# Kernel optimization log

Measured on AMD Instinct MI355X. Metric: run time of the kernel, lower is better.

The kernel has to match this reference:

```python
import math
import jax, jax.numpy as jnp
import numpy as np

N_ORDERS = 2
CHUNK = 64  # tokens per chunk (before virtual-token expansion)


def _expand_derivative(x, n):
    """expand_virtual_tokens(mode='derivative'): [B,H,S,D] -> [B,H,S*n,D]."""
    B, H, S, D = x.shape
    pad = jnp.zeros((B, H, n - 1, D), x.dtype)
    xp = jnp.concatenate([pad, x], axis=2)  # [B,H,S+n-1,D]
    coeffs = np.array([(-1) ** kk * math.comb(n - 1, kk) for kk in range(n)], dtype=np.float32)
    coeffs = coeffs / np.abs(coeffs).sum()  # L1-normalized binomial coeffs
    # window j at token t is x_pad[t+j]*coeffs[j]; then flip window dim (as in torch .flip(-1))
    win = jnp.stack([xp[:, :, j:j + S, :] * coeffs[j] for j in range(n)], axis=3)  # [B,H,S,n,D]
    win = win[:, :, :, ::-1, :]
    return win.reshape(B, H, S * n, D)


def _unlinear(x, scale=2.0):
    """unlinear_activation: gated norm-scaled gelu applied to inter-chunk state."""
    xn = jnp.linalg.norm(x, axis=-1, keepdims=True) + 1e-6
    return x / scale * jax.nn.gelu(scale * x / xn, approximate=True)


def _stab(x):
    # ensure_stability: clamp to [-1e4, 1e4], nan -> center (0)
    return jnp.nan_to_num(jnp.clip(x, -1e4, 1e4), nan=0.0, posinf=1e4, neginf=-1e4)


def _forward(q, k, v, beta):
    n = N_ORDERS
    B, H, S, D = q.shape
    qe = _expand_derivative(q, n)
    ke = _expand_derivative(k, n)
    ve = _expand_derivative(v, n)
    be = jnp.repeat(beta, n, axis=-1)[..., None]  # [B,H,S*n,1]
    w = ke * be  # delta-rule write keys
    u = ve * be  # delta-rule write values

    Cn = CHUNK * n                     # virtual tokens per chunk
    NC = (S * n) // Cn                 # number of chunks
    ch = lambda x: x.reshape(B, H, NC, Cn, D)
    qc, kc, wc, uc = ch(qe), ch(ke), ch(w), ch(u)

    # triangular (forward-substitution) inversion per chunk:
    # T = (I + tril(W K^T, -1))^{-1}  == fast_invert_matrix of the strictly-lower system
    A = jnp.tril(jnp.einsum('bhnid,bhnjd->bhnij', wc, kc), -1)
    eye = jnp.eye(Cn, dtype=q.dtype)
    T = jax.scipy.linalg.solve_triangular(
        eye + A, jnp.broadcast_to(eye, A.shape), lower=True, unit_diagonal=True)
    wci = jnp.einsum('bhnij,bhnjd->bhnid', T, wc)
    uci = jnp.einsum('bhnij,bhnjd->bhnid', T, uc)

    def chunk_step(h, xs):
        # sequential_delta_product_scan body: per-token Householder updates, n_orders steps
        qx, wx, ux = xs  # each [B,H,Cn,D]
        C = CHUNK
        qr = qx.reshape(B, H, C, n, D)
        wr = wx.reshape(B, H, C, n, D)
        ur = ux.reshape(B, H, C, n, D)
        state = jnp.broadcast_to(h[:, :, None], (B, H, C, D, D))  # per-token state
        outs = []
        for s in range(n):
            qs, ws, us = qr[:, :, :, s], wr[:, :, :, s], ur[:, :, :, s]
            kho = jnp.einsum('bhcd,bhcde->bhce', ws, state)
            uval = us - kho
            o_inter = jnp.einsum('bhcd,bhcde->bhce', qs, state)
            o_intra = qs * uval
            state = _stab(state + jnp.einsum('bhcd,bhce->bhcde', ws, uval))
            outs.append(o_intra + o_inter)
        o = jnp.stack(outs, axis=3).reshape(B, H, C * n, D)  # interleave: pos t*n+s
        h_new = _unlinear(state[:, :, -1])  # linear_activation=False path
        return h_new, o

    xs = (jnp.moveaxis(qc, 2, 0), jnp.moveaxis(wci, 2, 0), jnp.moveaxis(uci, 2, 0))
    h0 = jnp.zeros((B, H, D, D), q.dtype)
    _, os = jax.lax.scan(chunk_step, h0, xs)  # os: [NC,B,H,Cn,D]
    out_v = jnp.moveaxis(os, 0, 2).reshape(B, H, S, n, D)
    return out_v[..., n - 1, :]  # collapse virtual tokens: keep last-order output per token


def setup_inputs() -> dict:
    key = jax.random.key(0)
    kq, kk, kv, kb = jax.random.split(key, 4)
    B, H, S, D = 2, 16, 2048, 64
    return {
        'q': jax.random.normal(kq, (B, H, S, D), jnp.float32),
        'k': jax.random.normal(kk, (B, H, S, D), jnp.float32),
        'v': jax.random.normal(kv, (B, H, S, D), jnp.float32),
        'beta': jax.random.uniform(kb, (B, H, S), jnp.float32),
    }


def reference(q, k, v, beta):
    return _forward(q, k, v, beta)
```

## Files before the change

### kernel.cpp

```cpp
#include <hip/hip_runtime.h>
#include <math.h>


namespace {
constexpr int PAIRS = 32;
constexpr int SLEN  = 2048;
constexpr int D     = 64;
constexpr int CK    = 64;
constexpr int CN    = 128;
constexpr int NCH   = 32;
constexpr int NB2   = 16;
constexpr int NP    = 5;
constexpr size_t YWORDS = (size_t)PAIRS * NCH * CN * CN;
constexpr int GP = 2145;
constexpr size_t GGW = (size_t)PAIRS * NCH * GP;
constexpr size_t HGW = (size_t)PAIRS * (NCH + 1) * D * D;

__device__ __forceinline__ float stab1(float x) {
    float y = __builtin_amdgcn_fmed3f(x, -10000.f, 10000.f);
    return (x != x) ? 0.f : y;
}

__device__ __forceinline__ int kidx(int a, int f4) {
    return a * 68 + 4 * (f4 ^ ((a >> 2) & 3));
}

__device__ __forceinline__ void bar_lds() {
    asm volatile("s_waitcnt lgkmcnt(0)\n\ts_barrier" ::: "memory");
}
}

__global__ __launch_bounds__(256, 2)
void la_gram(const float* __restrict__ kg, float* __restrict__ gG)
{
    __shared__ float kstf[65 * 68];
    const int blk = blockIdx.x;
    const int p = blk >> 5, nc = blk & 31;
    const int tid = threadIdx.x;
    const int baseT = nc * CK;
    const float* kp = kg + (size_t)p * SLEN * D;

    for (int u = tid; u < 65 * 16; u += 256) {
        int a = u >> 4, f4 = u & 15;
        int src = baseT - 1 + a;
        float4 val = float4{0.f, 0.f, 0.f, 0.f};
        if (src >= 0) val = ((const float4*)(kp + (size_t)src * D))[f4];
        *(float4*)&kstf[kidx(a, f4)] = val;
    }
    __syncthreads();

    float* gps = gG + (size_t)blk * GP;
    for (int tt = tid; tt < 17 * 17; tt += 256) {
        int ta = tt / 17, tb = tt % 17;
        if (tb > ta) continue;
        int a0 = ta * 4, b0 = tb * 4;
        float acc[4][4] = {};
        for (int d4 = 0; d4 < 16; ++d4) {
            float4 av[4], bv[4];
            #pragma unroll
            for (int r = 0; r < 4; ++r) {
                av[r] = *(const float4*)&kstf[kidx(min(a0 + r, 64), d4)];
                bv[r] = *(const float4*)&kstf[kidx(min(b0 + r, 64), d4)];
            }
            #pragma unroll
            for (int r = 0; r < 4; ++r)
                #pragma unroll
                for (int c = 0; c < 4; ++c)
                    acc[r][c] += av[r].x * bv[c].x + av[r].y * bv[c].y
                               + av[r].z * bv[c].z + av[r].w * bv[c].w;
        }
        #pragma unroll
        for (int r = 0; r < 4; ++r)
            #pragma unroll
            for (int c = 0; c < 4; ++c) {
                int a = a0 + r, b = b0 + c;
                if (a <= 64 && b <= a)
                    gps[a * (a + 1) / 2 + b] = acc[r][c];
            }
    }
}

__global__ __launch_bounds__(256, 3)
void la_phase1g(const float* __restrict__ kg, const float* __restrict__ vg,
                const float* __restrict__ bg, float* __restrict__ ws,
                const float* __restrict__ gG)
{
    __shared__ float Ysh[CN][64];
    __shared__ float scm[2][CN][8];
    __shared__ float redsh[24][66];
    __shared__ float bq4[CK], bh[CK];

    const int blk  = blockIdx.x;
    const int p    = blk >> 6;
    const int nc   = (blk >> 1) & 31;
    const int half = blk & 1;
    const int tid  = threadIdx.x;
    const int col  = tid & 63;
    const int m    = tid >> 6;
    const int baseT = nc * CK;
    const float* kp = kg + (size_t)p * SLEN * D;
    const float* vp = vg + (size_t)p * SLEN * D;
    const float* bp = bg + (size_t)p * SLEN;
    const float* gps = gG + (size_t)(p * NCH + nc) * GP;

    if (tid < CK) {
        float bv = bp[baseT + tid];
        bq4[tid] = 0.25f * bv;
        bh[tid]  = 0.5f  * bv;
    }
    __syncthreads();

    const float* srcBase = half ? vp : kp;
    for (int u = tid; u < CN * 16; u += 256) {
        int i = u >> 4, f4 = u & 15;
        int ci = i >> 1, si = i & 1;
        float sc = si ? bh[ci] : -bh[ci];
        int srcT = baseT + ci - si;
        float4 val = float4{0.f, 0.f, 0.f, 0.f};
        if (srcT >= 0) val = ((const float4*)(srcBase + (size_t)srcT * D))[f4];
        val.x *= sc; val.y *= sc; val.z *= sc; val.w *= sc;
        *(float4*)&Ysh[i][f4 * 4] = val;
    }
    for (int e = tid; e < 64; e += 256) {
        int j = e >> 3, r = e & 7;
        int ai = (r >> 1) - (r & 1) + 1;
        int aj = (j >> 1) - (j & 1) + 1;
        int amax = max(ai, aj), amin = min(ai, aj);
        float sgn = ((r ^ j) & 1) ? -1.f : 1.f;
        scm[0][j][r] = sgn * bq4[r >> 1] * gps[amax * (amax + 1) / 2 + amin];
    }
    __syncthreads();

    #pragma unroll
    for (int g = 0; g < 16; ++g) {
        const int buf = g & 1;
        float acc[8] = {};
        #pragma unroll
        for (int jj = 0; jj < 2 * g; ++jj) {
            const int j = m + 4 * jj;
            float yv = Ysh[j][col];
            const float4 a03 = *(const float4*)&scm[buf][j][0];
            const float4 a47 = *(const float4*)&scm[buf][j][4];
            acc[0] += a03.x * yv; acc[1] += a03.y * yv;
            acc[2] += a03.z * yv; acc[3] += a03.w * yv;
            acc[4] += a47.x * yv; acc[5] += a47.y * yv;
            acc[6] += a47.z * yv; acc[7] += a47.w * yv;
        }
        if (m > 0) {
            #pragma unroll
            for (int r = 0; r < 8; ++r) redsh[(m - 1) * 8 + r][col] = acc[r];
        }
        bar_lds();
        if (m == 0) {
            if (g > 0) {
                #pragma unroll
                for (int r = 0; r < 8; ++r)
                    acc[r] += redsh[r][col] + redsh[8 + r][col] + redsh[16 + r][col];
            }
            float yn[8];
            #pragma unroll
            for (int r = 0; r < 8; ++r) {
                float val = Ysh[8 * g + r][col] - acc[r];
                #pragma unroll
                for (int rp = 0; rp < 8; ++rp)
                    if (rp < r) val -= scm[buf][8 * g + rp][r] * yn[rp];
                yn[r] = val;
                Ysh[8 * g + r][col] = val;
            }
        } else if (g < 15) {
            const int T = g + 1, bufB = T & 1;
            const int nel = 8 * (8 * T + 8);
            constexpr int MAXIT = 6;
            const int nit = (nel + 191) / 192;
            #pragma unroll
            for (int it = 0; it < MAXIT; ++it) {
                if (it < nit) {
                    const int e = (tid - 64) + 192 * it;
                    if (e < nel) {
                        int j = e >> 3, r = e & 7;
                        int i = 8 * T + r;
                        int ai = (i >> 1) - (i & 1) + 1;
                        int aj = (j >> 1) - (j & 1) + 1;
                        int amax = max(ai, aj), amin = min(ai, aj);
                        float sgn = ((i ^ j) & 1) ? -1.f : 1.f;
                        scm[bufB][j][r] =
                            sgn * bq4[i >> 1] * gps[amax * (amax + 1) / 2 + amin];
                    }
                }
            }
        }
        bar_lds();
    }

    float* gY = ws + (size_t)(p * NCH + nc) * (CN * CN) + half * 64;
    for (int u = tid; u < CN * 16; u += 256) {
        int r = u >> 4, f4 = u & 15;
        *(float4*)&gY[r * CN + f4 * 4] = *(const float4*)&Ysh[r][f4 * 4];
    }
}

__global__ __launch_bounds__(512, 1)
void la_scan(const float* __restrict__ ws, float* __restrict__ hg)
{
    __shared__ float w0s[64], u0s[64], w1s[64], u1s[64];
    __shared__ float pA[8][64], pB[8][64];
    __shared__ float hsh2[64][67];

    const int p = blockIdx.x;
    const int tid = threadIdx.x;
    const int w = tid >> 6, lane = tid & 63;
    const int hd = tid >> 3, he0 = (tid & 7) * 8;
    const float* Yp = ws + (size_t)p * NCH * (CN * CN);
    float* hp = hg + (size_t)p * (NCH + 1) * (D * D);

    for (int idx = tid; idx < D * D; idx += 512) hp[idx] = 0.f;
    for (int idx = tid; idx < 64 * 67; idx += 512) (&hsh2[0][0])[idx] = 0.f;

    auto stagew = [&](float v) {
        if (tid < 64)       w0s[tid] = v;
        else if (tid < 128) u0s[tid - 64] = v;
        else if (tid < 192) w1s[tid - 128] = v;
        else if (tid < 256) u1s[tid - 192] = v;
    };
    {
        float v = 0.f;
        if (tid < 256) v = Yp[(size_t)(126 + (tid >> 7)) * CN + (tid & 127)];
        stagew(v);
    }
    float hs[8];
    #pragma unroll
    for (int j = 0; j < 8; ++j) hs[j] = 0.f;
    __syncthreads();

    for (int nc = 0; nc < NCH; ++nc) {
        float pf = 0.f;
        if (nc + 1 < NCH && tid < 256)
            pf = Yp[(size_t)(nc + 1) * (CN * CN)
                    + (size_t)(126 + (tid >> 7)) * CN + (tid & 127)];

        float s = 0.f;
        #pragma unroll
        for (int j = 0; j < 8; ++j) s += w0s[8 * w + j] * hs[j];
        pA[w][lane] = s;
        bar_lds();

        float sum = 0.f;
        #pragma unroll
        for (int wv = 0; wv < 8; ++wv) sum += pA[wv][lane];
        const float uv0 = u0s[lane] - sum;

        float st1[8];
        float s2 = 0.f;
        #pragma unroll
        for (int j = 0; j < 8; ++j) {
            st1[j] = stab1(hs[j] + w0s[8 * w + j] * uv0);
            s2 += w1s[8 * w + j] * st1[j];
        }
        pB[w][lane] = s2;
        bar_lds();

        float sum2 = 0.f;
        #pragma unroll
        for (int wv = 0; wv < 8; ++wv) sum2 += pB[wv][lane];
        const float uv1 = u1s[lane] - sum2;
        #pragma unroll
        for (int j = 0; j < 8; ++j)
            hsh2[8 * w + j][lane] = stab1(st1[j] + w1s[8 * w + j] * uv1);
        bar_lds();

        {
            float st2v[8];
            float ssum = 0.f;
            #pragma unroll
            for (int j = 0; j < 8; ++j) {
                st2v[j] = hsh2[hd][he0 + j];
                ssum += st2v[j] * st2v[j];
            }
            ssum += __shfl_xor(ssum, 1);
            ssum += __shfl_xor(ssum, 2);
            ssum += __shfl_xor(ssum, 4);
            float xn = __builtin_amdgcn_sqrtf(ssum) + 1e-6f;
            float sc2 = 2.f * __builtin_amdgcn_rcpf(xn);
            float hn[8];
            #pragma unroll
            for (int j = 0; j < 8; ++j) {
                float x  = st2v[j];
                float y  = x * sc2;
                float y2 = y * y;
                float e  = __builtin_amdgcn_exp2f(y * (2.3022078f + 0.1029432f * y2));
                float th = (e - 1.f) * __builtin_amdgcn_rcpf(e + 1.f);
                hn[j] = 0.25f * x * y * (1.f + th);
                hsh2[hd][he0 + j] = hn[j];
            }
            float* ho = hp + (size_t)(nc + 1) * (D * D) + hd * 64 + he0;
            *(float4*)&ho[0] = float4{hn[0], hn[1], hn[2], hn[3]};
            *(float4*)&ho[4] = float4{hn[4], hn[5], hn[6], hn[7]};
        }
        if (nc + 1 < NCH) stagew(pf);
        bar_lds();
        #pragma unroll
        for (int j = 0; j < 8; ++j) hs[j] = hsh2[8 * w + j][lane];
    }
}

__global__ __launch_bounds__(512)
void la_out(const float* __restrict__ qg, const float* __restrict__ ws,
            const float* __restrict__ hg, float* __restrict__ outg)
{
    __shared__ float hT[64 * 68];
    __shared__ float wbr[8][3][64];

    const int blk = blockIdx.x;
    const int p = blk >> 5, nc = blk & 31;
    const int tid = threadIdx.x;
    const int w = tid >> 6, lane = tid & 63;

    const float* Yc = ws + (size_t)(p * NCH + nc) * (CN * CN);
    const float* hp = hg + ((size_t)p * (NCH + 1) + nc) * (D * D);
    const float* qp = qg + (size_t)p * SLEN * D;
    float* op = outg + (size_t)p * SLEN * D;

    for (int idx = tid; idx < D * D; idx += 512) {
        int d = idx >> 6, e = idx & 63;
        hT[e * 68 + d] = hp[idx];
    }
    __syncthreads();

    float4 hr[16];
    #pragma unroll
    for (int k = 0; k < 16; ++k)
        hr[k] = *(const float4*)&hT[lane * 68 + 4 * k];

    float w0n, u0n, w1n, u1n, qn;
    {
        const int c = w, t = nc * CK + c;
        w0n = Yc[(size_t)(2 * c) * CN + lane];
        u0n = Yc[(size_t)(2 * c) * CN + 64 + lane];
        w1n = Yc[(size_t)(2 * c + 1) * CN + lane];
        u1n = Yc[(size_t)(2 * c + 1) * CN + 64 + lane];
        qn  = qp[(size_t)((t > 0) ? t - 1 : 0) * D + lane];
    }

    for (int it = 0; it < 8; ++it) {
        const int c = it * 8 + w;
        const int t = nc * CK + c;
        const float w0v = w0n, u0l = u0n, w1v = w1n, u1l = u1n, qv = qn;
        if (it < 7) {
            const int c2 = (it + 1) * 8 + w;
            w0n = Yc[(size_t)(2 * c2) * CN + lane];
            u0n = Yc[(size_t)(2 * c2) * CN + 64 + lane];
            w1n = Yc[(size_t)(2 * c2 + 1) * CN + lane];
            u1n = Yc[(size_t)(2 * c2 + 1) * CN + 64 + lane];
            qn  = qp[(size_t)(nc * CK + c2 - 1) * D + lane];
        }

        wbr[w][0][lane] = w0v;
        wbr[w][1][lane] = w1v;
        wbr[w][2][lane] = qv;

        float uv0 = u0l;
        #pragma unroll
        for (int k = 0; k < 16; ++k) {
            float4 wb = *(const float4*)&wbr[w][0][4 * k];
            uv0 -= (wb.x * hr[k].x + wb.y * hr[k].y)
                 + (wb.z * hr[k].z + wb.w * hr[k].w);
        }
        float kh = 0.f, oa = 0.f;
        #pragma unroll
        for (int k = 0; k < 16; ++k) {
            float4 wb0 = *(const float4*)&wbr[w][0][4 * k];
            float4 wb1 = *(const float4*)&wbr[w][1][4 * k];
            float4 qb  = *(const float4*)&wbr[w][2][4 * k];
            float st0 = stab1(hr[k].x + wb0.x * uv0);
            float st1 = stab1(hr[k].y + wb0.y * uv0);
            float st2 = stab1(hr[k].z + wb0.z * uv0);
            float st3 = stab1(hr[k].w + wb0.w * uv0);
            kh += (wb1.x * st0 + wb1.y * st1) + (wb1.z * st2 + wb1.w * st3);
            oa += (qb.x * st0 + qb.y * st1) + (qb.z * st2 + qb.w * st3);
        }
        float uv1 = u1l - kh;
        float outv = 0.5f * (qv * uv1 + oa);
        op[(size_t)t * D + lane] = (t > 0) ? outv : 0.f;
    }
}

__global__ __launch_bounds__(256, 2)
void la_phase1f(const float* __restrict__ kg, const float* __restrict__ vg,
                const float* __restrict__ bg, float* __restrict__ ws)
{
    __shared__ float Ysh[CN][64];
    __shared__ float Gm[65][66];
    __shared__ char  ureg[17680];
    __shared__ float bq4[CK], bh[CK];

    float* kstf = (float*)ureg;
    float* scm  = (float*)ureg;
    float (*redsh)[66] = (float(*)[66])(ureg + 8192);

    const int blk  = blockIdx.x;
    const int p    = blk >> 6;
    const int nc   = (blk >> 1) & 31;
    const int half = blk & 1;
    const int tid  = threadIdx.x;
    const int baseT = nc * CK;
    const float* kp = kg + (size_t)p * SLEN * D;
    const float* vp = vg + (size_t)p * SLEN * D;
    const float* bp = bg + (size_t)p * SLEN;

    for (int u = tid; u < 65 * 16; u += 256) {
        int a = u >> 4, f4 = u & 15;
        int src = baseT - 1 + a;
        float4 val = float4{0.f, 0.f, 0.f, 0.f};
        if (src >= 0) val = ((const float4*)(kp + (size_t)src * D))[f4];
        *(float4*)&kstf[kidx(a, f4)] = val;
    }
    if (tid < CK) {
        float bv = bp[baseT + tid];
        bq4[tid] = 0.25f * bv;
        bh[tid]  = 0.5f  * bv;
    }
    __syncthreads();

    for (int u = tid; u < CN * 16; u += 256) {
        int i = u >> 4, f4 = u & 15;
        int ci = i >> 1, si = i & 1;
        float sc = si ? bh[ci] : -bh[ci];
        float4 val = float4{0.f, 0.f, 0.f, 0.f};
        if (half == 0) {
            val = *(const float4*)&kstf[kidx(ci - si + 1, f4)];
        } else {
            int srcT = baseT + ci - si;
            if (srcT >= 0) val = ((const float4*)(vp + (size_t)srcT * D))[f4];
        }
        val.x *= sc; val.y *= sc; val.z *= sc; val.w *= sc;
        *(float4*)&Ysh[i][f4 * 4] = val;
    }

    for (int tt = tid; tt < 17 * 17; tt += 256) {
        int ta = tt / 17, tb = tt % 17;
        if (tb > ta) continue;
        int a0 = ta * 4, b0 = tb * 4;
        float acc[4][4] = {};
        for (int d4 = 0; d4 < 16; ++d4) {
            float4 av[4], bv[4];
            #pragma unroll
            for (int r = 0; r < 4; ++r) {
                av[r] = *(const float4*)&kstf[kidx(min(a0 + r, 64), d4)];
                bv[r] = *(const float4*)&kstf[kidx(min(b0 + r, 64), d4)];
            }
            #pragma unroll
            for (int r = 0; r < 4; ++r)
                #pragma unroll
                for (int c = 0; c < 4; ++c)
                    acc[r][c] += av[r].x * bv[c].x + av[r].y * bv[c].y
                               + av[r].z * bv[c].z + av[r].w * bv[c].w;
        }
        #pragma unroll
        for (int r = 0; r < 4; ++r)
            #pragma unroll
            for (int c = 0; c < 4; ++c)
                if (a0 + r <= 64 && b0 + c <= 64) {
                    Gm[a0 + r][b0 + c] = acc[r][c];
                    Gm[b0 + c][a0 + r] = acc[r][c];
                }
    }
    __syncthreads();

    auto stripf = [&](int g, int t0, int tstride) {
        int buf = g & 1;
        int jmax = 8 * g + 8;
        for (int e = t0; e < 8 * jmax; e += tstride) {
            int j = e >> 3, r = e & 7;
            int i = 8 * g + r;
            int ai = (i >> 1) - (i & 1) + 1;
            int aj = (j >> 1) - (j & 1) + 1;
            float sgn = ((i ^ j) & 1) ? -1.f : 1.f;
            scm[(buf * CN + j) * 8 + r] = sgn * bq4[i >> 1] * Gm[ai][aj];
        }
    };

    stripf(0, tid, 256);
    __syncthreads();

    const int col = tid & 63;
    const int m   = tid >> 6;
    for (int g = 0; g < 16; ++g) {
        const int buf = g & 1;
        float acc[8] = {};
        for (int j = m; j < 8 * g; j += 4) {
            float yv = Ysh[j][col];
            const float4 a03 = *(const float4*)&scm[(buf * CN + j) * 8];
            const float4 a47 = *(const float4*)&scm[(buf * CN + j) * 8 + 4];
            acc[0] += a03.x * yv; acc[1] += a03.y * yv;
            acc[2] += a03.z * yv; acc[3] += a03.w * yv;
            acc[4] += a47.x * yv; acc[5] += a47.y * yv;
            acc[6] += a47.z * yv; acc[7] += a47.w * yv;
        }
        if (m > 0) {
            #pragma unroll
            for (int r = 0; r < 8; ++r) redsh[(m - 1) * 8 + r][col] = acc[r];
        }
        __syncthreads();
        if (m == 0) {
            if (g > 0) {
                #pragma unroll
                for (int r = 0; r < 8; ++r)
                    acc[r] += redsh[r][col] + redsh[8 + r][col] + redsh[16 + r][col];
            }
            float yn[8];
            #pragma unroll
            for (int r = 0; r < 8; ++r) {
                float val = Ysh[8 * g + r][col] - acc[r];
                #pragma unroll
                for (int rp = 0; rp < 8; ++rp)
                    if (rp < r) val -= scm[(buf * CN + 8 * g + rp) * 8 + r] * yn[rp];
                yn[r] = val;
                Ysh[8 * g + r][col] = val;
            }
        } else if (g < 15) {
            stripf(g + 1, tid - 64, 192);
        }
        __syncthreads();
    }

    float* gY = ws + (size_t)(p * NCH + nc) * (CN * CN) + half * 64;
    for (int u = tid; u < CN * 16; u += 256) {
        int r = u >> 4, f4 = u & 15;
        *(float4*)&gY[r * CN + f4 * 4] = *(const float4*)&Ysh[r][f4 * 4];
    }
}

__global__ __launch_bounds__(512, 4)
void la_phase2(const float* __restrict__ qg, const float* __restrict__ ws,
               float* __restrict__ outg)
{
    __shared__ float WU[2][NP][256];
    __shared__ float Qs[2][NP][64];
    __shared__ float pR1[8][NP][64];
    __shared__ float pKH[8][NP][64];
    __shared__ float pOA[8][NP][64];
    __shared__ float UV0[NP][64];
    __shared__ float UV1r[64];
    __shared__ float hsh[64][67];

    const int blk  = blockIdx.x;
    const int p    = blk >> 4, nb = blk & 15;
    const int tid  = threadIdx.x;
    const int w    = tid >> 6, lane = tid & 63;
    const int hd   = tid >> 3;
    const int he0  = (tid & 7) * 8;

    const float* qp = qg + (size_t)p * SLEN * D;
    float* op = outg + (size_t)p * SLEN * D;
    const float* wsbase = ws + (size_t)p * NCH * (CN * CN);

    const int cMain = nb * 4 + w;

    float4 wuR = float4{0.f, 0.f, 0.f, 0.f};
    float  qR  = 0.f;

    auto stage_load = [&](int nc) {
        const float* gY = wsbase + (size_t)nc * (CN * CN);
        if (w < 4) {
            wuR = *(const float4*)(gY + (size_t)(2 * cMain) * CN + lane * 4);
            int t = nc * CK + cMain;
            qR = qp[(size_t)((t > 0) ? t - 1 : 0) * D + lane];
        } else if (w == 4) {
            wuR = *(const float4*)(gY + (size_t)126 * CN + lane * 4);
            qR = qp[(size_t)(nc * CK + 62) * D + lane];
        }
    };
    auto stage_write = [&](int buf) {
        if (w < NP) {
            *(float4*)&WU[buf][w][lane * 4] = wuR;
            Qs[buf][w][lane] = qR;
        }
    };

    for (int idx = tid; idx < 64 * 67; idx += 512) (&hsh[0][0])[idx] = 0.f;
    stage_load(0);
    stage_write(0);
    __syncthreads();

    for (int nc = 0; nc < NCH; ++nc) {
        const int buf = nc & 1;
        float hs[8];
        #pragma unroll
        for (int j = 0; j < 8; ++j) hs[j] = hsh[8 * w + j][lane];
        if (nc + 1 < NCH) stage_load(nc + 1);

        #pragma unroll
        for (int P = 0; P < NP; ++P) {
            float4 a = *(const float4*)&WU[buf][P][8 * w];
            float4 b = *(const float4*)&WU[buf][P][8 * w + 4];
            pR1[w][P][lane] =
                  ((a.x * hs[0] + a.y * hs[1]) + (a.z * hs[2] + a.w * hs[3]))
                + ((b.x * hs[4] + b.y * hs[5]) + (b.z * hs[6] + b.w * hs[7]));
        }
        __syncthreads();

        if (w < NP) {
            float s = 0.f;
            #pragma unroll
            for (int wv = 0; wv < 8; ++wv) s += pR1[wv][w][lane];
            UV0[w][lane] = WU[buf][w][64 + lane] - s;
        }
        __syncthreads();

        #pragma unroll
        for (int P = 0; P < NP; ++P) {
            float uv0 = UV0[P][lane];
            float4 w0a = *(const float4*)&WU[buf][P][8 * w];
            float4 w0b = *(const float4*)&WU[buf][P][8 * w + 4];
            float4 w1a = *(const float4*)&WU[buf][P][128 + 8 * w];
            float4 w1b = *(const float4*)&WU[buf][P][128 + 8 * w + 4];
            float4 qa  = *(const float4*)&Qs[buf][P][8 * w];
            float4 qb  = *(const float4*)&Qs[buf][P][8 * w + 4];
            float st0 = stab1(hs[0] + w0a.x * uv0);
            float st1 = stab1(hs[1] + w0a.y * uv0);
            float st2 = stab1(hs[2] + w0a.z * uv0);
            float st3 = stab1(hs[3] + w0a.w * uv0);
            float st4 = stab1(hs[4] + w0b.x * uv0);
            float st5 = stab1(hs[5] + w0b.y * uv0);
            float st6 = stab1(hs[6] + w0b.z * uv0);
            float st7 = stab1(hs[7] + w0b.w * uv0);
            pKH[w][P][lane] =
                  ((w1a.x * st0 + w1a.y * st1) + (w1a.z * st2 + w1a.w * st3))
                + ((w1b.x * st4 + w1b.y * st5) + (w1b.z * st6 + w1b.w * st7));
            pOA[w][P][lane] =
                  ((qa.x * st0 + qa.y * st1) + (qa.z * st2 + qa.w * st3))
                + ((qb.x * st4 + qb.y * st5) + (qb.z * st6 + qb.w * st7));
        }
        stage_write(buf ^ 1);
        __syncthreads();

        if (w < 4) {
            float skh = 0.f, soa = 0.f;
            #pragma unroll
            for (int wv = 0; wv < 8; ++wv) {
                skh += pKH[wv][w][lane];
                soa += pOA[wv][w][lane];
            }
            float uv1 = WU[buf][w][192 + lane] - skh;
            int t = nc * CK + cMain;
            float outv = 0.5f * (Qs[buf][w][lane] * uv1 + soa);
            op[(size_t)t * D + lane] = (t > 0) ? outv : 0.f;
        } else if (w == 4) {
            float skh = 0.f;
            #pragma unroll
            for (int wv = 0; wv < 8; ++wv) skh += pKH[wv][4][lane];
            UV1r[lane] = WU[buf][4][192 + lane] - skh;
        }
        __syncthreads();

        {
            float w0d = WU[buf][4][hd];
            float w1d = WU[buf][4][128 + hd];
            float st2v[8];
            float ssum = 0.f;
            #pragma unroll
            for (int j = 0; j < 8; ++j) {
                float st1 = stab1(hsh[hd][he0 + j] + w0d * UV0[4][he0 + j]);
                float st2 = stab1(st1 + w1d * UV1r[he0 + j]);
                st2v[j] = st2;
                ssum += st2 * st2;
            }
            ssum += __shfl_xor(ssum, 1);
            ssum += __shfl_xor(ssum, 2);
            ssum += __shfl_xor(ssum, 4);
            float xn = __builtin_amdgcn_sqrtf(ssum) + 1e-6f;
            float s2 = 2.f * __builtin_amdgcn_rcpf(xn);
            #pragma unroll
            for (int j = 0; j < 8; ++j) {
                float x  = st2v[j];
                float y  = x * s2;
                float y2 = y * y;
                float e  = __builtin_amdgcn_exp2f(y * (2.3022078f + 0.1029432f * y2));
                float th = (e - 1.f) * __builtin_amdgcn_rcpf(e + 1.f);
                hsh[hd][he0 + j] = 0.25f * x * y * (1.f + th);
            }
        }
        __syncthreads();
    }
}

extern "C" void kernel_launch(void* const* d_in, const int* in_sizes, int n_in,
                              void* d_out, int out_size, void* d_ws, size_t ws_size,
                              hipStream_t stream)
{
    (void)in_sizes; (void)n_in; (void)out_size;
    const float* q    = (const float*)d_in[0];
    const float* k    = (const float*)d_in[1];
    const float* v    = (const float*)d_in[2];
    const float* beta = (const float*)d_in[3];
    float* ws  = (float*)d_ws;
    float* out = (float*)d_out;

    const size_t maxW  = (HGW > GGW) ? HGW : GGW;
    const size_t needA = (YWORDS + maxW) * sizeof(float);
    const size_t needB = (YWORDS + GGW) * sizeof(float);

    if (ws_size >= needA) {
        float* gG = ws + YWORDS;
        float* hg = ws + YWORDS;
        la_gram<<<PAIRS * NCH, 256, 0, stream>>>(k, gG);
        la_phase1g<<<PAIRS * NCH * 2, 256, 0, stream>>>(k, v, beta, ws, gG);
        la_scan<<<PAIRS, 512, 0, stream>>>(ws, hg);
        la_out<<<PAIRS * NCH, 512, 0, stream>>>(q, ws, hg, out);
    } else if (ws_size >= needB) {
        float* gG = ws + YWORDS;
        la_gram<<<PAIRS * NCH, 256, 0, stream>>>(k, gG);
        la_phase1g<<<PAIRS * NCH * 2, 256, 0, stream>>>(k, v, beta, ws, gG);
        la_phase2<<<PAIRS * NB2, 512, 0, stream>>>(q, ws, out);
    } else {
        la_phase1f<<<PAIRS * NCH * 2, 256, 0, stream>>>(k, v, beta, ws);
        la_phase2<<<PAIRS * NB2, 512, 0, stream>>>(q, ws, out);
    }
}
```

Measured before the change: 260.5 us.

## Fuse per-chunk solve and inter-chunk scan into one kernel with flag handoff

Merges the chunk-wise triangular solve (phase1g) and the sequential state scan into a single launch. The first PAIRS blocks run the scan and spin on per-chunk atomic flags, while the remaining blocks compute chunk Y matrices (ordered by chunk index) and signal completion with release atomics. This lets the serial scan start as soon as early chunks are ready instead of waiting for the whole phase, and drops one kernel launch. In exchange it adds a memset, relies on scan blocks being co-resident with producers to avoid deadlock, and runs the scan with 256 threads instead of 512.

```diff
diff --git a/kernel.cpp b/kernel.cpp
--- a/kernel.cpp
+++ b/kernel.cpp
@@ -15,16 +15,15 @@
 constexpr int GP = 2145;
 constexpr size_t GGW = (size_t)PAIRS * NCH * GP;
 constexpr size_t HGW = (size_t)PAIRS * (NCH + 1) * D * D;
+constexpr size_t FLW = PAIRS * NCH;
 
 __device__ __forceinline__ float stab1(float x) {
     float y = __builtin_amdgcn_fmed3f(x, -10000.f, 10000.f);
     return (x != x) ? 0.f : y;
 }
-
 __device__ __forceinline__ int kidx(int a, int f4) {
     return a * 68 + 4 * (f4 ^ ((a >> 2) & 3));
 }
-
 __device__ __forceinline__ void bar_lds() {
     asm volatile("s_waitcnt lgkmcnt(0)\n\ts_barrier" ::: "memory");
 }
@@ -81,20 +80,128 @@
 }
 
 __global__ __launch_bounds__(256, 3)
-void la_phase1g(const float* __restrict__ kg, const float* __restrict__ vg,
-                const float* __restrict__ bg, float* __restrict__ ws,
-                const float* __restrict__ gG)
+void la_p1scan(const float* __restrict__ kg, const float* __restrict__ vg,
+               const float* __restrict__ bg, float* __restrict__ ws,
+               const float* __restrict__ gG, float* __restrict__ hg,
+               unsigned int* __restrict__ flags)
 {
-    __shared__ float Ysh[CN][64];
-    __shared__ float scm[2][CN][8];
-    __shared__ float redsh[24][66];
-    __shared__ float bq4[CK], bh[CK];
-
-    const int blk  = blockIdx.x;
-    const int p    = blk >> 6;
-    const int nc   = (blk >> 1) & 31;
-    const int half = blk & 1;
-    const int tid  = threadIdx.x;
+    __shared__ char shm[47808];
+    const int blk = blockIdx.x;
+    const int tid = threadIdx.x;
+
+    if (blk < PAIRS) {
+        float* w0s = (float*)shm;
+        float* u0s = w0s + 64;
+        float* w1s = u0s + 64;
+        float* u1s = w1s + 64;
+        float (*pA)[64] = (float(*)[64])(u1s + 64);
+        float (*pB)[64] = pA + 4;
+        float (*hsh2)[67] = (float(*)[67])(pB + 4);
+
+        const int p = blk;
+        const int w = tid >> 6, lane = tid & 63;
+        const int hd = tid >> 2, he0 = (tid & 3) * 16;
+        const float* Yp = ws + (size_t)p * NCH * (CN * CN);
+        float* hp = hg + (size_t)p * (NCH + 1) * (D * D);
+        const unsigned int* fl = (const unsigned int*)flags + (size_t)p * NCH;
+
+        for (int idx = tid; idx < D * D; idx += 256) hp[idx] = 0.f;
+
+        float hs[16];
+        #pragma unroll
+        for (int j = 0; j < 16; ++j) hs[j] = 0.f;
+
+        for (int nc = 0; nc < NCH; ++nc) {
+            if (tid == 0) {
+                while (__hip_atomic_load(&fl[nc], __ATOMIC_ACQUIRE,
+                                         __HIP_MEMORY_SCOPE_AGENT) < 2u)
+                    __builtin_amdgcn_s_sleep(16);
+            }
+            __syncthreads();
+
+            {
+                float v = Yp[(size_t)nc * (CN * CN)
+                             + (size_t)(126 + (tid >> 7)) * CN + (tid & 127)];
+                if (tid < 64)       w0s[tid] = v;
+                else if (tid < 128) u0s[tid - 64] = v;
+                else if (tid < 192) w1s[tid - 128] = v;
+                else                u1s[tid - 192] = v;
+            }
+            bar_lds();
+
+            float s = 0.f;
+            #pragma unroll
+            for (int j = 0; j < 16; ++j) s += w0s[16 * w + j] * hs[j];
+            pA[w][lane] = s;
+            bar_lds();
+
+            float sum = pA[0][lane] + pA[1][lane] + pA[2][lane] + pA[3][lane];
+            const float uv0 = u0s[lane] - sum;
+
+            float st1[16];
+            float s2 = 0.f;
+            #pragma unroll
+            for (int j = 0; j < 16; ++j) {
+                st1[j] = stab1(hs[j] + w0s[16 * w + j] * uv0);
+                s2 += w1s[16 * w + j] * st1[j];
+            }
+            pB[w][lane] = s2;
+            bar_lds();
+
+            float sum2 = pB[0][lane] + pB[1][lane] + pB[2][lane] + pB[3][lane];
+            const float uv1 = u1s[lane] - sum2;
+            #pragma unroll
+            for (int j = 0; j < 16; ++j)
+                hsh2[16 * w + j][lane] = stab1(st1[j] + w1s[16 * w + j] * uv1);
+            bar_lds();
+
+            {
+                float st2v[16];
+                float ssum = 0.f;
+                #pragma unroll
+                for (int j = 0; j < 16; ++j) {
+                    st2v[j] = hsh2[hd][he0 + j];
+                    ssum += st2v[j] * st2v[j];
+                }
+                ssum += __shfl_xor(ssum, 1);
+                ssum += __shfl_xor(ssum, 2);
+                float xn = __builtin_amdgcn_sqrtf(ssum) + 1e-6f;
+                float sc2 = 2.f * __builtin_amdgcn_rcpf(xn);
+                float* ho = hp + (size_t)(nc + 1) * (D * D) + hd * 64 + he0;
+                #pragma unroll
+                for (int j4 = 0; j4 < 4; ++j4) {
+                    float hn[4];
+                    #pragma unroll
+                    for (int q = 0; q < 4; ++q) {
+                        float x  = st2v[4 * j4 + q];
+                        float y  = x * sc2;
+                        float y2 = y * y;
+                        float e  = __builtin_amdgcn_exp2f(
+                                       y * (2.3022078f + 0.1029432f * y2));
+                        float th = (e - 1.f) * __builtin_amdgcn_rcpf(e + 1.f);
+                        hn[q] = 0.25f * x * y * (1.f + th);
+                        hsh2[hd][he0 + 4 * j4 + q] = hn[q];
+                    }
+                    *(float4*)&ho[4 * j4] = float4{hn[0], hn[1], hn[2], hn[3]};
+                }
+            }
+            bar_lds();
+            #pragma unroll
+            for (int j = 0; j < 16; ++j) hs[j] = hsh2[16 * w + j][lane];
+        }
+        return;
+    }
+
+    float (*Ysh)[64]   = (float(*)[64])shm;
+    float (*scm)[CN][8] = (float(*)[CN][8])(shm + 32768);
+    float (*redsh)[66] = (float(*)[66])(shm + 40960);
+    float* bq4 = (float*)(shm + 47296);
+    float* bh  = bq4 + 64;
+
+    const int idx  = blk - PAIRS;
+    const int nc   = idx >> 6;
+    const int p    = (idx & 63) >> 1;
+    const int half = idx & 1;
     const int col  = tid & 63;
     const int m    = tid >> 6;
     const int baseT = nc * CK;
@@ -197,110 +304,10 @@
         int r = u >> 4, f4 = u & 15;
         *(float4*)&gY[r * CN + f4 * 4] = *(const float4*)&Ysh[r][f4 * 4];
     }
-}
-
-__global__ __launch_bounds__(512, 1)
-void la_scan(const float* __restrict__ ws, float* __restrict__ hg)
-{
-    __shared__ float w0s[64], u0s[64], w1s[64], u1s[64];
-    __shared__ float pA[8][64], pB[8][64];
-    __shared__ float hsh2[64][67];
-
-    const int p = blockIdx.x;
-    const int tid = threadIdx.x;
-    const int w = tid >> 6, lane = tid & 63;
-    const int hd = tid >> 3, he0 = (tid & 7) * 8;
-    const float* Yp = ws + (size_t)p * NCH * (CN * CN);
-    float* hp = hg + (size_t)p * (NCH + 1) * (D * D);
-
-    for (int idx = tid; idx < D * D; idx += 512) hp[idx] = 0.f;
-    for (int idx = tid; idx < 64 * 67; idx += 512) (&hsh2[0][0])[idx] = 0.f;
-
-    auto stagew = [&](float v) {
-        if (tid < 64)       w0s[tid] = v;
-        else if (tid < 128) u0s[tid - 64] = v;
-        else if (tid < 192) w1s[tid - 128] = v;
-        else if (tid < 256) u1s[tid - 192] = v;
-    };
-    {
-        float v = 0.f;
-        if (tid < 256) v = Yp[(size_t)(126 + (tid >> 7)) * CN + (tid & 127)];
-        stagew(v);
-    }
-    float hs[8];
-    #pragma unroll
-    for (int j = 0; j < 8; ++j) hs[j] = 0.f;
-    __syncthreads();
-
-    for (int nc = 0; nc < NCH; ++nc) {
-        float pf = 0.f;
-        if (nc + 1 < NCH && tid < 256)
-            pf = Yp[(size_t)(nc + 1) * (CN * CN)
-                    + (size_t)(126 + (tid >> 7)) * CN + (tid & 127)];
-
-        float s = 0.f;
-        #pragma unroll
-        for (int j = 0; j < 8; ++j) s += w0s[8 * w + j] * hs[j];
-        pA[w][lane] = s;
-        bar_lds();
-
-        float sum = 0.f;
-        #pragma unroll
-        for (int wv = 0; wv < 8; ++wv) sum += pA[wv][lane];
-        const float uv0 = u0s[lane] - sum;
-
-        float st1[8];
-        float s2 = 0.f;
-        #pragma unroll
-        for (int j = 0; j < 8; ++j) {
-            st1[j] = stab1(hs[j] + w0s[8 * w + j] * uv0);
-            s2 += w1s[8 * w + j] * st1[j];
-        }
-        pB[w][lane] = s2;
-        bar_lds();
-
-        float sum2 = 0.f;
-        #pragma unroll
-        for (int wv = 0; wv < 8; ++wv) sum2 += pB[wv][lane];
-        const float uv1 = u1s[lane] - sum2;
-        #pragma unroll
-        for (int j = 0; j < 8; ++j)
-            hsh2[8 * w + j][lane] = stab1(st1[j] + w1s[8 * w + j] * uv1);
-        bar_lds();
-
-        {
-            float st2v[8];
-            float ssum = 0.f;
-            #pragma unroll
-            for (int j = 0; j < 8; ++j) {
-                st2v[j] = hsh2[hd][he0 + j];
-                ssum += st2v[j] * st2v[j];
-            }
-            ssum += __shfl_xor(ssum, 1);
-            ssum += __shfl_xor(ssum, 2);
-            ssum += __shfl_xor(ssum, 4);
-            float xn = __builtin_amdgcn_sqrtf(ssum) + 1e-6f;
-            float sc2 = 2.f * __builtin_amdgcn_rcpf(xn);
-            float hn[8];
-            #pragma unroll
-            for (int j = 0; j < 8; ++j) {
-                float x  = st2v[j];
-                float y  = x * sc2;
-                float y2 = y * y;
-                float e  = __builtin_amdgcn_exp2f(y * (2.3022078f + 0.1029432f * y2));
-                float th = (e - 1.f) * __builtin_amdgcn_rcpf(e + 1.f);
-                hn[j] = 0.25f * x * y * (1.f + th);
-                hsh2[hd][he0 + j] = hn[j];
-            }
-            float* ho = hp + (size_t)(nc + 1) * (D * D) + hd * 64 + he0;
-            *(float4*)&ho[0] = float4{hn[0], hn[1], hn[2], hn[3]};
-            *(float4*)&ho[4] = float4{hn[4], hn[5], hn[6], hn[7]};
-        }
-        if (nc + 1 < NCH) stagew(pf);
-        bar_lds();
-        #pragma unroll
-        for (int j = 0; j < 8; ++j) hs[j] = hsh2[8 * w + j][lane];
-    }
+    __syncthreads();
+    if (tid == 0)
+        __hip_atomic_fetch_add(&flags[p * NCH + nc], 1u, __ATOMIC_RELEASE,
+                               __HIP_MEMORY_SCOPE_AGENT);
 }
 
 __global__ __launch_bounds__(512)
@@ -381,6 +388,229 @@
         float uv1 = u1l - kh;
         float outv = 0.5f * (qv * uv1 + oa);
         op[(size_t)t * D + lane] = (t > 0) ? outv : 0.f;
+    }
+}
+
+__global__ __launch_bounds__(256, 3)
+void la_phase1g(const float* __restrict__ kg, const float* __restrict__ vg,
+                const float* __restrict__ bg, float* __restrict__ ws,
+                const float* __restrict__ gG)
+{
+    __shared__ float Ysh[CN][64];
+    __shared__ float scm[2][CN][8];
+    __shared__ float redsh[24][66];
+    __shared__ float bq4[CK], bh[CK];
+
+    const int blk  = blockIdx.x;
+    const int p    = blk >> 6;
+    const int nc   = (blk >> 1) & 31;
+    const int half = blk & 1;
+    const int tid  = threadIdx.x;
+    const int col  = tid & 63;
+    const int m    = tid >> 6;
+    const int baseT = nc * CK;
+    const float* kp = kg + (size_t)p * SLEN * D;
+    const float* vp = vg + (size_t)p * SLEN * D;
+    const float* bp = bg + (size_t)p * SLEN;
+    const float* gps = gG + (size_t)(p * NCH + nc) * GP;
+
+    if (tid < CK) {
+        float bv = bp[baseT + tid];
+        bq4[tid] = 0.25f * bv;
+        bh[tid]  = 0.5f  * bv;
+    }
+    __syncthreads();
+
+    const float* srcBase = half ? vp : kp;
+    for (int u = tid; u < CN * 16; u += 256) {
+        int i = u >> 4, f4 = u & 15;
+        int ci = i >> 1, si = i & 1;
+        float sc = si ? bh[ci] : -bh[ci];
+        int srcT = baseT + ci - si;
+        float4 val = float4{0.f, 0.f, 0.f, 0.f};
+        if (srcT >= 0) val = ((const float4*)(srcBase + (size_t)srcT * D))[f4];
+        val.x *= sc; val.y *= sc; val.z *= sc; val.w *= sc;
+        *(float4*)&Ysh[i][f4 * 4] = val;
+    }
+    for (int e = tid; e < 64; e += 256) {
+        int j = e >> 3, r = e & 7;
+        int ai = (r >> 1) - (r & 1) + 1;
+        int aj = (j >> 1) - (j & 1) + 1;
+        int amax = max(ai, aj), amin = min(ai, aj);
+        float sgn = ((r ^ j) & 1) ? -1.f : 1.f;
+        scm[0][j][r] = sgn * bq4[r >> 1] * gps[amax * (amax + 1) / 2 + amin];
+    }
+    __syncthreads();
+
+    #pragma unroll
+    for (int g = 0; g < 16; ++g) {
+        const int buf = g & 1;
+        float acc[8] = {};
+        #pragma unroll
+        for (int jj = 0; jj < 2 * g; ++jj) {
+            const int j = m + 4 * jj;
+            float yv = Ysh[j][col];
+            const float4 a03 = *(const float4*)&scm[buf][j][0];
+            const float4 a47 = *(const float4*)&scm[buf][j][4];
+            acc[0] += a03.x * yv; acc[1] += a03.y * yv;
+            acc[2] += a03.z * yv; acc[3] += a03.w * yv;
+            acc[4] += a47.x * yv; acc[5] += a47.y * yv;
+            acc[6] += a47.z * yv; acc[7] += a47.w * yv;
+        }
+        if (m > 0) {
+            #pragma unroll
+            for (int r = 0; r < 8; ++r) redsh[(m - 1) * 8 + r][col] = acc[r];
+        }
+        bar_lds();
+        if (m == 0) {
+            if (g > 0) {
+                #pragma unroll
+                for (int r = 0; r < 8; ++r)
+                    acc[r] += redsh[r][col] + redsh[8 + r][col] + redsh[16 + r][col];
+            }
+            float yn[8];
+            #pragma unroll
+            for (int r = 0; r < 8; ++r) {
+                float val = Ysh[8 * g + r][col] - acc[r];
+                #pragma unroll
+                for (int rp = 0; rp < 8; ++rp)
+                    if (rp < r) val -= scm[buf][8 * g + rp][r] * yn[rp];
+                yn[r] = val;
+                Ysh[8 * g + r][col] = val;
+            }
+        } else if (g < 15) {
+            const int T = g + 1, bufB = T & 1;
+            const int nel = 8 * (8 * T + 8);
+            constexpr int MAXIT = 6;
+            const int nit = (nel + 191) / 192;
+            #pragma unroll
+            for (int it = 0; it < MAXIT; ++it) {
+                if (it < nit) {
+                    const int e = (tid - 64) + 192 * it;
+                    if (e < nel) {
+                        int j = e >> 3, r = e & 7;
+                        int i = 8 * T + r;
+                        int ai = (i >> 1) - (i & 1) + 1;
+                        int aj = (j >> 1) - (j & 1) + 1;
+                        int amax = max(ai, aj), amin = min(ai, aj);
+                        float sgn = ((i ^ j) & 1) ? -1.f : 1.f;
+                        scm[bufB][j][r] =
+                            sgn * bq4[i >> 1] * gps[amax * (amax + 1) / 2 + amin];
+                    }
+                }
+            }
+        }
+        bar_lds();
+    }
+
+    float* gY = ws + (size_t)(p * NCH + nc) * (CN * CN) + half * 64;
+    for (int u = tid; u < CN * 16; u += 256) {
+        int r = u >> 4, f4 = u & 15;
+        *(float4*)&gY[r * CN + f4 * 4] = *(const float4*)&Ysh[r][f4 * 4];
+    }
+}
+
+__global__ __launch_bounds__(512, 1)
+void la_scan(const float* __restrict__ ws, float* __restrict__ hg)
+{
+    __shared__ float w0s[64], u0s[64], w1s[64], u1s[64];
+    __shared__ float pA[8][64], pB[8][64];
+    __shared__ float hsh2[64][67];
+
+    const int p = blockIdx.x;
+    const int tid = threadIdx.x;
+    const int w = tid >> 6, lane = tid & 63;
+    const int hd = tid >> 3, he0 = (tid & 7) * 8;
+    const float* Yp = ws + (size_t)p * NCH * (CN * CN);
+    float* hp = hg + (size_t)p * (NCH + 1) * (D * D);
+
+    for (int idx = tid; idx < D * D; idx += 512) hp[idx] = 0.f;
+    for (int idx = tid; idx < 64 * 67; idx += 512) (&hsh2[0][0])[idx] = 0.f;
+
+    auto stagew = [&](float v) {
+        if (tid < 64)       w0s[tid] = v;
+        else if (tid < 128) u0s[tid - 64] = v;
+        else if (tid < 192) w1s[tid - 128] = v;
+        else if (tid < 256) u1s[tid - 192] = v;
+    };
+    {
+        float v = 0.f;
+        if (tid < 256) v = Yp[(size_t)(126 + (tid >> 7)) * CN + (tid & 127)];
+        stagew(v);
+    }
+    float hs[8];
+    #pragma unroll
+    for (int j = 0; j < 8; ++j) hs[j] = 0.f;
+    __syncthreads();
+
+    for (int nc = 0; nc < NCH; ++nc) {
+        float pf = 0.f;
+        if (nc + 1 < NCH && tid < 256)
+            pf = Yp[(size_t)(nc + 1) * (CN * CN)
+                    + (size_t)(126 + (tid >> 7)) * CN + (tid & 127)];
+
+        float s = 0.f;
+        #pragma unroll
+        for (int j = 0; j < 8; ++j) s += w0s[8 * w + j] * hs[j];
+        pA[w][lane] = s;
+        bar_lds();
+
+        float sum = 0.f;
+        #pragma unroll
+        for (int wv = 0; wv < 8; ++wv) sum += pA[wv][lane];
+        const float uv0 = u0s[lane] - sum;
+
+        float st1[8];
+        float s2 = 0.f;
+        #pragma unroll
+        for (int j = 0; j < 8; ++j) {
+            st1[j] = stab1(hs[j] + w0s[8 * w + j] * uv0);
+            s2 += w1s[8 * w + j] * st1[j];
+        }
+        pB[w][lane] = s2;
+        bar_lds();
+
+        float sum2 = 0.f;
+        #pragma unroll
+        for (int wv = 0; wv < 8; ++wv) sum2 += pB[wv][lane];
+        const float uv1 = u1s[lane] - sum2;
+        #pragma unroll
+        for (int j = 0; j < 8; ++j)
+            hsh2[8 * w + j][lane] = stab1(st1[j] + w1s[8 * w + j] * uv1);
+        bar_lds();
+
+        {
+            float st2v[8];
+            float ssum = 0.f;
+            #pragma unroll
+            for (int j = 0; j < 8; ++j) {
+                st2v[j] = hsh2[hd][he0 + j];
+                ssum += st2v[j] * st2v[j];
+            }
+            ssum += __shfl_xor(ssum, 1);
+            ssum += __shfl_xor(ssum, 2);
+            ssum += __shfl_xor(ssum, 4);
+            float xn = __builtin_amdgcn_sqrtf(ssum) + 1e-6f;
+            float sc2 = 2.f * __builtin_amdgcn_rcpf(xn);
+            float hn[8];
+            #pragma unroll
+            for (int j = 0; j < 8; ++j) {
+                float x  = st2v[j];
+                float y  = x * sc2;
+                float y2 = y * y;
+                float e  = __builtin_amdgcn_exp2f(y * (2.3022078f + 0.1029432f * y2));
+                float th = (e - 1.f) * __builtin_amdgcn_rcpf(e + 1.f);
+                hn[j] = 0.25f * x * y * (1.f + th);
+                hsh2[hd][he0 + j] = hn[j];
+            }
+            float* ho = hp + (size_t)(nc + 1) * (D * D) + hd * 64 + he0;
+            *(float4*)&ho[0] = float4{hn[0], hn[1], hn[2], hn[3]};
+            *(float4*)&ho[4] = float4{hn[4], hn[5], hn[6], hn[7]};
+        }
+        if (nc + 1 < NCH) stagew(pf);
+        bar_lds();
+        #pragma unroll
+        for (int j = 0; j < 8; ++j) hs[j] = hsh2[8 * w + j][lane];
     }
 }
 
@@ -697,10 +927,20 @@
     float* out = (float*)d_out;
 
     const size_t maxW  = (HGW > GGW) ? HGW : GGW;
+    const size_t needF = (YWORDS + GGW + HGW + FLW) * sizeof(float);
     const size_t needA = (YWORDS + maxW) * sizeof(float);
     const size_t needB = (YWORDS + GGW) * sizeof(float);
 
-    if (ws_size >= needA) {
+    if (ws_size >= needF) {
+        float* gG = ws + YWORDS;
+        float* hg = gG + GGW;
+        unsigned int* flags = (unsigned int*)(hg + HGW);
+        hipMemsetAsync(flags, 0, FLW * sizeof(unsigned int), stream);
+        la_gram<<<PAIRS * NCH, 256, 0, stream>>>(k, gG);
+        la_p1scan<<<PAIRS + PAIRS * NCH * 2, 256, 0, stream>>>(
+            k, v, beta, ws, gG, hg, (unsigned int*)flags);
+        la_out<<<PAIRS * NCH, 512, 0, stream>>>(q, ws, hg, out);
+    } else if (ws_size >= needA) {
         float* gG = ws + YWORDS;
         float* hg = ws + YWORDS;
         la_gram<<<PAIRS * NCH, 256, 0, stream>>>(k, gG);
```

After: 292.7 us. 12.3% more time.

## Fuse scan and output kernels with per-chunk flags to overlap them

Applied to the files above, without the earlier changes.

The sequential state scan and the per-chunk output computation are merged into one launch. The first 32 blocks run the scan and publish a release flag after each chunk's state is written. The remaining blocks spin on an acquire load of their chunk's flag before reading that state. Output work for early chunks can now overlap the serial scan instead of waiting for the whole scan kernel to finish. In exchange the change adds a memset launch and spin-waiting, and it relies on the scan blocks being scheduled before or alongside the waiting blocks to avoid deadlock.

```diff
diff --git a/kernel.cpp b/kernel.cpp
--- a/kernel.cpp
+++ b/kernel.cpp
@@ -15,16 +15,15 @@
 constexpr int GP = 2145;
 constexpr size_t GGW = (size_t)PAIRS * NCH * GP;
 constexpr size_t HGW = (size_t)PAIRS * (NCH + 1) * D * D;
+constexpr size_t FLW2 = (size_t)PAIRS * NCH;
 
 __device__ __forceinline__ float stab1(float x) {
     float y = __builtin_amdgcn_fmed3f(x, -10000.f, 10000.f);
     return (x != x) ? 0.f : y;
 }
-
 __device__ __forceinline__ int kidx(int a, int f4) {
     return a * 68 + 4 * (f4 ^ ((a >> 2) & 3));
 }
-
 __device__ __forceinline__ void bar_lds() {
     asm volatile("s_waitcnt lgkmcnt(0)\n\ts_barrier" ::: "memory");
 }
@@ -199,126 +198,148 @@
     }
 }
 
-__global__ __launch_bounds__(512, 1)
-void la_scan(const float* __restrict__ ws, float* __restrict__ hg)
+__global__ __launch_bounds__(512)
+void la_scanout(const float* __restrict__ qg, const float* __restrict__ ws,
+                float* __restrict__ hg, float* __restrict__ outg,
+                unsigned int* __restrict__ flags)
 {
-    __shared__ float w0s[64], u0s[64], w1s[64], u1s[64];
-    __shared__ float pA[8][64], pB[8][64];
-    __shared__ float hsh2[64][67];
-
-    const int p = blockIdx.x;
+    __shared__ char shm[23808];
+    const int blk = blockIdx.x;
     const int tid = threadIdx.x;
-    const int w = tid >> 6, lane = tid & 63;
-    const int hd = tid >> 3, he0 = (tid & 7) * 8;
-    const float* Yp = ws + (size_t)p * NCH * (CN * CN);
-    float* hp = hg + (size_t)p * (NCH + 1) * (D * D);
-
-    for (int idx = tid; idx < D * D; idx += 512) hp[idx] = 0.f;
-    for (int idx = tid; idx < 64 * 67; idx += 512) (&hsh2[0][0])[idx] = 0.f;
-
-    auto stagew = [&](float v) {
-        if (tid < 64)       w0s[tid] = v;
-        else if (tid < 128) u0s[tid - 64] = v;
-        else if (tid < 192) w1s[tid - 128] = v;
-        else if (tid < 256) u1s[tid - 192] = v;
-    };
-    {
-        float v = 0.f;
-        if (tid < 256) v = Yp[(size_t)(126 + (tid >> 7)) * CN + (tid & 127)];
-        stagew(v);
-    }
-    float hs[8];
-    #pragma unroll
-    for (int j = 0; j < 8; ++j) hs[j] = 0.f;
-    __syncthreads();
-
-    for (int nc = 0; nc < NCH; ++nc) {
-        float pf = 0.f;
-        if (nc + 1 < NCH && tid < 256)
-            pf = Yp[(size_t)(nc + 1) * (CN * CN)
-                    + (size_t)(126 + (tid >> 7)) * CN + (tid & 127)];
-
-        float s = 0.f;
-        #pragma unroll
-        for (int j = 0; j < 8; ++j) s += w0s[8 * w + j] * hs[j];
-        pA[w][lane] = s;
-        bar_lds();
-
-        float sum = 0.f;
-        #pragma unroll
-        for (int wv = 0; wv < 8; ++wv) sum += pA[wv][lane];
-        const float uv0 = u0s[lane] - sum;
-
-        float st1[8];
-        float s2 = 0.f;
-        #pragma unroll
-        for (int j = 0; j < 8; ++j) {
-            st1[j] = stab1(hs[j] + w0s[8 * w + j] * uv0);
-            s2 += w1s[8 * w + j] * st1[j];
-        }
-        pB[w][lane] = s2;
-        bar_lds();
-
-        float sum2 = 0.f;
-        #pragma unroll
-        for (int wv = 0; wv < 8; ++wv) sum2 += pB[wv][lane];
-        const float uv1 = u1s[lane] - sum2;
-        #pragma unroll
-        for (int j = 0; j < 8; ++j)
-            hsh2[8 * w + j][lane] = stab1(st1[j] + w1s[8 * w + j] * uv1);
-        bar_lds();
-
+
+    if (blk < PAIRS) {
+        float* w0s = (float*)shm;
+        float* u0s = w0s + 64;
+        float* w1s = u0s + 64;
+        float* u1s = w1s + 64;
+        float (*pA)[64] = (float(*)[64])(u1s + 64);
+        float (*pB)[64] = pA + 8;
+        float (*hsh2)[67] = (float(*)[67])(pB + 8);
+
+        const int p = blk;
+        const int w = tid >> 6, lane = tid & 63;
+        const int hd = tid >> 3, he0 = (tid & 7) * 8;
+        const float* Yp = ws + (size_t)p * NCH * (CN * CN);
+        float* hp = hg + (size_t)p * (NCH + 1) * (D * D);
+        unsigned int* fl = flags + (size_t)p * NCH;
+
+        for (int idx = tid; idx < D * D; idx += 512) hp[idx] = 0.f;
+        for (int idx = tid; idx < 64 * 67; idx += 512) (&hsh2[0][0])[idx] = 0.f;
+
+        auto stagew = [&](float v) {
+            if (tid < 64)       w0s[tid] = v;
+            else if (tid < 128) u0s[tid - 64] = v;
+            else if (tid < 192) w1s[tid - 128] = v;
+            else if (tid < 256) u1s[tid - 192] = v;
+        };
         {
-            float st2v[8];
-            float ssum = 0.f;
+            float v = 0.f;
+            if (tid < 256) v = Yp[(size_t)(126 + (tid >> 7)) * CN + (tid & 127)];
+            stagew(v);
+        }
+        float hs[8];
+        #pragma unroll
+        for (int j = 0; j < 8; ++j) hs[j] = 0.f;
+        __syncthreads();
+        if (tid == 0)
+            __hip_atomic_fetch_add(&fl[0], 1u, __ATOMIC_RELEASE,
+                                   __HIP_MEMORY_SCOPE_AGENT);
+
+        for (int nc = 0; nc < NCH; ++nc) {
+            float pf = 0.f;
+            if (nc + 1 < NCH && tid < 256)
+                pf = Yp[(size_t)(nc + 1) * (CN * CN)
+                        + (size_t)(126 + (tid >> 7)) * CN + (tid & 127)];
+
+            float s = 0.f;
+            #pragma unroll
+            for (int j = 0; j < 8; ++j) s += w0s[8 * w + j] * hs[j];
+            pA[w][lane] = s;
+            bar_lds();
+
+            float sum = 0.f;
+            #pragma unroll
+            for (int wv = 0; wv < 8; ++wv) sum += pA[wv][lane];
+            const float uv0 = u0s[lane] - sum;
+
+            float st1[8];
+            float s2 = 0.f;
             #pragma unroll
             for (int j = 0; j < 8; ++j) {
-                st2v[j] = hsh2[hd][he0 + j];
-                ssum += st2v[j] * st2v[j];
-            }
-            ssum += __shfl_xor(ssum, 1);
-            ssum += __shfl_xor(ssum, 2);
-            ssum += __shfl_xor(ssum, 4);
-            float xn = __builtin_amdgcn_sqrtf(ssum) + 1e-6f;
-            float sc2 = 2.f * __builtin_amdgcn_rcpf(xn);
-            float hn[8];
-            #pragma unroll
-            for (int j = 0; j < 8; ++j) {
-                float x  = st2v[j];
-                float y  = x * sc2;
-                float y2 = y * y;
-                float e  = __builtin_amdgcn_exp2f(y * (2.3022078f + 0.1029432f * y2));
-                float th = (e - 1.f) * __builtin_amdgcn_rcpf(e + 1.f);
-                hn[j] = 0.25f * x * y * (1.f + th);
-                hsh2[hd][he0 + j] = hn[j];
-            }
-            float* ho = hp + (size_t)(nc + 1) * (D * D) + hd * 64 + he0;
-            *(float4*)&ho[0] = float4{hn[0], hn[1], hn[2], hn[3]};
-            *(float4*)&ho[4] = float4{hn[4], hn[5], hn[6], hn[7]};
-        }
-        if (nc + 1 < NCH) stagew(pf);
-        bar_lds();
-        #pragma unroll
-        for (int j = 0; j < 8; ++j) hs[j] = hsh2[8 * w + j][lane];
-    }
-}
-
-__global__ __launch_bounds__(512)
-void la_out(const float* __restrict__ qg, const float* __restrict__ ws,
-            const float* __restrict__ hg, float* __restrict__ outg)
-{
-    __shared__ float hT[64 * 68];
-    __shared__ float wbr[8][3][64];
-
-    const int blk = blockIdx.x;
-    const int p = blk >> 5, nc = blk & 31;
-    const int tid = threadIdx.x;
+                st1[j] = stab1(hs[j] + w0s[8 * w + j] * uv0);
+                s2 += w1s[8 * w + j] * st1[j];
+            }
+            pB[w][lane] = s2;
+            bar_lds();
+
+            float sum2 = 0.f;
+            #pragma unroll
+            for (int wv = 0; wv < 8; ++wv) sum2 += pB[wv][lane];
+            const float uv1 = u1s[lane] - sum2;
+            #pragma unroll
+            for (int j = 0; j < 8; ++j)
+                hsh2[8 * w + j][lane] = stab1(st1[j] + w1s[8 * w + j] * uv1);
+            bar_lds();
+
+            {
+                float st2v[8];
+                float ssum = 0.f;
+                #pragma unroll
+                for (int j = 0; j < 8; ++j) {
+                    st2v[j] = hsh2[hd][he0 + j];
+                    ssum += st2v[j] * st2v[j];
+                }
+                ssum += __shfl_xor(ssum, 1);
+                ssum += __shfl_xor(ssum, 2);
+                ssum += __shfl_xor(ssum, 4);
+                float xn = __builtin_amdgcn_sqrtf(ssum) + 1e-6f;
+                float sc2 = 2.f * __builtin_amdgcn_rcpf(xn);
+                float hn[8];
+                #pragma unroll
+                for (int j = 0; j < 8; ++j) {
+                    float x  = st2v[j];
+                    float y  = x * sc2;
+                    float y2 = y * y;
+                    float e  = __builtin_amdgcn_exp2f(
+                                   y * (2.3022078f + 0.1029432f * y2));
+                    float th = (e - 1.f) * __builtin_amdgcn_rcpf(e + 1.f);
+                    hn[j] = 0.25f * x * y * (1.f + th);
+                    hsh2[hd][he0 + j] = hn[j];
+                }
+                float* ho = hp + (size_t)(nc + 1) * (D * D) + hd * 64 + he0;
+                *(float4*)&ho[0] = float4{hn[0], hn[1], hn[2], hn[3]};
+                *(float4*)&ho[4] = float4{hn[4], hn[5], hn[6], hn[7]};
+            }
+            if (nc + 1 < NCH) stagew(pf);
+            __syncthreads();
+            if (tid == 0 && nc + 1 < NCH)
+                __hip_atomic_fetch_add(&fl[nc + 1], 1u, __ATOMIC_RELEASE,
+                                       __HIP_MEMORY_SCOPE_AGENT);
+            #pragma unroll
+            for (int j = 0; j < 8; ++j) hs[j] = hsh2[8 * w + j][lane];
+        }
+        return;
+    }
+
+    float* hT = (float*)shm;
+    float (*wbr)[3][64] = (float(*)[3][64])(hT + 64 * 68);
+
+    const int idx2 = blk - PAIRS;
+    const int p = idx2 >> 5, nc = idx2 & 31;
     const int w = tid >> 6, lane = tid & 63;
 
     const float* Yc = ws + (size_t)(p * NCH + nc) * (CN * CN);
     const float* hp = hg + ((size_t)p * (NCH + 1) + nc) * (D * D);
     const float* qp = qg + (size_t)p * SLEN * D;
     float* op = outg + (size_t)p * SLEN * D;
+
+    if (tid == 0) {
+        const unsigned int* fl = flags + (size_t)p * NCH;
+        while (__hip_atomic_load(&fl[nc], __ATOMIC_ACQUIRE,
+                                 __HIP_MEMORY_SCOPE_AGENT) < 1u)
+            __builtin_amdgcn_s_sleep(16);
+    }
+    __syncthreads();
 
     for (int idx = tid; idx < D * D; idx += 512) {
         int d = idx >> 6, e = idx & 63;
@@ -696,17 +717,18 @@
     float* ws  = (float*)d_ws;
     float* out = (float*)d_out;
 
-    const size_t maxW  = (HGW > GGW) ? HGW : GGW;
-    const size_t needA = (YWORDS + maxW) * sizeof(float);
+    const size_t reg2  = (HGW > GGW) ? HGW : GGW;
+    const size_t needF = (YWORDS + reg2 + FLW2) * sizeof(float);
     const size_t needB = (YWORDS + GGW) * sizeof(float);
 
-    if (ws_size >= needA) {
+    if (ws_size >= needF) {
         float* gG = ws + YWORDS;
         float* hg = ws + YWORDS;
+        unsigned int* flags = (unsigned int*)(ws + YWORDS + reg2);
+        hipMemsetAsync(flags, 0, FLW2 * sizeof(unsigned int), stream);
         la_gram<<<PAIRS * NCH, 256, 0, stream>>>(k, gG);
         la_phase1g<<<PAIRS * NCH * 2, 256, 0, stream>>>(k, v, beta, ws, gG);
-        la_scan<<<PAIRS, 512, 0, stream>>>(ws, hg);
-        la_out<<<PAIRS * NCH, 512, 0, stream>>>(q, ws, hg, out);
+        la_scanout<<<PAIRS + PAIRS * NCH, 512, 0, stream>>>(q, ws, hg, out, flags);
     } else if (ws_size >= needB) {
         float* gG = ws + YWORDS;
         la_gram<<<PAIRS * NCH, 256, 0, stream>>>(k, gG);
```

New measurement: 341.9 us. 1.31x slower.
